# Kernel tuning notes

Measured on AMD Instinct MI355X. Metric: run time of the kernel, lower is better.

Reference implementation:

```python
import jax, jax.numpy as jnp
import numpy as np

CH = 128
DQK = CH // 8  # 16


def setup_inputs() -> dict:
    key = jax.random.key(0)
    ks = jax.random.split(key, 8)
    B, H, W, C = 4, 64, 64, CH
    inputs = jax.random.normal(ks[0], (B, H, W, C), dtype=jnp.float32)
    # 1x1 conv weights == dense over channel dim
    wq = jax.random.normal(ks[1], (C, DQK), dtype=jnp.float32) * (1.0 / np.sqrt(C))
    bq = jnp.zeros((DQK,), dtype=jnp.float32)
    wk = jax.random.normal(ks[2], (C, DQK), dtype=jnp.float32) * (1.0 / np.sqrt(C))
    bk = jnp.zeros((DQK,), dtype=jnp.float32)
    wv = jax.random.normal(ks[3], (C, C), dtype=jnp.float32) * (1.0 / np.sqrt(C))
    bv = jnp.zeros((C,), dtype=jnp.float32)
    gamma = jnp.zeros((1,), dtype=jnp.float32)
    return {"inputs": inputs, "wq": wq, "bq": bq, "wk": wk, "bk": bk,
            "wv": wv, "bv": bv, "gamma": gamma}


def reference(inputs, wq, bq, wk, bk, wv, bv, gamma):
    B, H, W, C = inputs.shape
    N = H * W
    x = inputs.reshape(B, N, C)  # flatten spatial
    q = x @ wq + bq              # [B, N, d]
    k = x @ wk + bk              # [B, N, d]
    v = x @ wv + bv              # [B, N, C]
    # full N x N attention (no scaling, per SAGAN source)
    scores = jnp.einsum('bnd,bmd->bnm', q, k)
    attn = jax.nn.softmax(scores, axis=-1)
    out = jnp.einsum('bnm,bmc->bnc', attn, v).reshape(B, H, W, C)
    return gamma * out + inputs
```

## Files before the change

kernel.cpp:

```cpp
#include <hip/hip_runtime.h>
#include <hip/hip_bf16.h>


typedef __attribute__((ext_vector_type(4)))  short short4v;
typedef __attribute__((ext_vector_type(8)))  short short8;
typedef __attribute__((ext_vector_type(16))) float f32x16;
typedef unsigned short u16;

#define LOG2E 1.4426950408889634f

__device__ __forceinline__ u16 f2bf(float f) {
  __hip_bfloat16 h = __float2bfloat16(f);
  return __builtin_bit_cast(u16, h);
}
__device__ __forceinline__ u16 f2bf_fast(float f) {
  unsigned u = __builtin_bit_cast(unsigned, f) + 0x8000u;
  return (u16)(u >> 16);
}
__device__ __forceinline__ float bf2f(u16 u) {
  unsigned v = (unsigned)u << 16;
  return __builtin_bit_cast(float, v);
}
__device__ __forceinline__ float fexp2(float x) {
#if __has_builtin(__builtin_amdgcn_exp2f)
  return __builtin_amdgcn_exp2f(x);
#else
  return exp2f(x);
#endif
}
__device__ __forceinline__ unsigned pkbf(float lo, float hi) {
  unsigned a = __builtin_bit_cast(unsigned, lo) + 0x8000u;
  unsigned b = __builtin_bit_cast(unsigned, hi) + 0x8000u;
  unsigned r;
  asm("v_perm_b32 %0, %1, %2, %3" : "=v"(r) : "v"(b), "v"(a), "s"(0x07060302u));
  return r;
}
__device__ __forceinline__ float xhalf_sum(float x) {
  float a = x, b = x;
  asm("v_permlane32_swap_b32 %0, %1" : "+v"(a), "+v"(b));
  return a + b;
}

__global__ __launch_bounds__(256) void qkv_proj(
    const float* __restrict__ x,
    const float* __restrict__ wq, const float* __restrict__ bq,
    const float* __restrict__ wk, const float* __restrict__ bk,
    const float* __restrict__ wv, const float* __restrict__ bv,
    u16* __restrict__ Qb, u16* __restrict__ Kb, u16* __restrict__ Vt)
{
  __shared__ u16 xs[128 * 136];
  __shared__ u16 ws[160 * 136];
  const int tid  = threadIdx.x;
  const int b    = blockIdx.x >> 6;
  const int n0   = ((blockIdx.x >> 1) & 31) * 128;
  const int half = blockIdx.x & 1;

  const float4* xg = (const float4*)(x + ((size_t)b * 4096 + n0) * 128);
#pragma unroll
  for (int p = 0; p < 16; ++p) {
    int idx = tid + p * 256;
    float4 v = xg[idx];
    int n = idx >> 5, i4 = idx & 31;
    short4v pk;
    pk[0] = (short)f2bf(v.x); pk[1] = (short)f2bf(v.y);
    pk[2] = (short)f2bf(v.z); pk[3] = (short)f2bf(v.w);
    *(short4v*)(xs + n * 136 + i4 * 4) = pk;
  }
  if (half == 0) {
#pragma unroll
    for (int p = 0; p < 8; ++p) {
      int idx = tid + p * 256;
      int k = idx >> 4, d = idx & 15;
      ws[d * 136 + k]        = f2bf(wq[idx] * LOG2E);
      ws[(16 + d) * 136 + k] = f2bf(wk[idx]);
    }
#pragma unroll
    for (int p = 0; p < 32; ++p) {
      int idx = tid + p * 256;
      int k = idx >> 6, c = idx & 63;
      ws[(32 + c) * 136 + k] = f2bf(wv[k * 128 + c]);
    }
  } else {
#pragma unroll
    for (int p = 0; p < 32; ++p) {
      int idx = tid + p * 256;
      int k = idx >> 6, c = 64 + (idx & 63);
      ws[(32 + c) * 136 + k] = f2bf(wv[k * 128 + c]);
    }
  }
  __syncthreads();

  const int lane = tid & 63, wid = tid >> 6;
  const int ln31 = lane & 31, hi = lane >> 5;
  const int NJ = half ? 2 : 3;

#pragma unroll 1
  for (int j = 0; j < NJ; ++j) {
    int t = wid + j * 4;
    int mt, nt;
    if (half == 0) { mt = t / 3; nt = t % 3; }
    else           { mt = t >> 1; nt = 3 + (t & 1); }
    const u16* arow = xs + (mt * 32 + ln31) * 136 + hi * 8;
    const u16* brow = ws + (nt * 32 + ln31) * 136 + hi * 8;
    f32x16 acc = (f32x16)0.0f;
#pragma unroll
    for (int ks = 0; ks < 8; ++ks) {
      short8 a = *(const short8*)(arow + ks * 16);
      short8 w = *(const short8*)(brow + ks * 16);
      acc = __builtin_amdgcn_mfma_f32_32x32x16_bf16(a, w, acc, 0, 0, 0);
    }
    if (nt == 0) {
      float bias = (ln31 < 16) ? bq[ln31] * LOG2E : bk[ln31 & 15];
      u16* base = ((ln31 < 16) ? Qb : Kb)
                + ((size_t)b * 4096 + n0 + mt * 32) * 16 + (ln31 & 15);
#pragma unroll
      for (int r = 0; r < 16; ++r) {
        int nl = (r & 3) + 8 * (r >> 2) + 4 * hi;
        base[nl * 16] = f2bf(acc[r] + bias);
      }
    } else {
      int c = (nt - 1) * 32 + ln31;
      float bias = bv[c];
      u16* vb = Vt + ((size_t)b * 128 + c) * 4096 + n0 + mt * 32 + 4 * hi;
#pragma unroll
      for (int g = 0; g < 4; ++g) {
        short4v pk;
        pk[0] = (short)f2bf(acc[g*4+0] + bias);
        pk[1] = (short)f2bf(acc[g*4+1] + bias);
        pk[2] = (short)f2bf(acc[g*4+2] + bias);
        pk[3] = (short)f2bf(acc[g*4+3] + bias);
        *(short4v*)(vb + 8 * g) = pk;
      }
    }
  }
}

template<int NKS>
__global__ __launch_bounds__(256, 3) void attn(
    const u16* __restrict__ Qb, const u16* __restrict__ Kb,
    const u16* __restrict__ Vt,
    u16* __restrict__ Ob, float* __restrict__ Lp)
{
  __shared__ __align__(16) char sm[2][18432];
  const int tid  = threadIdx.x;
  const int lane = tid & 63;
  const int wid  = tid >> 6;
  const int ln31 = lane & 31;
  const int hi   = lane >> 5;

  const int bx   = blockIdx.x;
  const int ks   = bx % NKS;
  const int rest = bx / NKS;
  const int b    = rest >> 5;
  const int qt   = rest & 31;
  const int qw   = qt * 128 + wid * 32;
  const int c0   = (ks * 64) / NKS;
  const int c1   = ((ks + 1) * 64) / NKS;

  const short8 qf = *(const short8*)(Qb + (((size_t)b * 4096 + qw + ln31) << 4) + (hi << 3));

  f32x16 acc[4];
#pragma unroll
  for (int ct = 0; ct < 4; ++ct) acc[ct] = (f32x16)0.0f;
  float lacc = 0.f;
  const f32x16 cbias = (f32x16)(-16.0f);

  const char* vg = (const char*)(Vt + (size_t)b * 128 * 4096);
  const char* kg = (const char*)(Kb + (size_t)b * 4096 * 16);
  const int vc = tid >> 1;
  const int vp = tid & 1;

  uint4 rv0, rv1, rv2, rv3;
  uint4 rk0, rk1;
  short8 paA0, paA1, paB0, paB1;

  auto loadV = [&](int kb) {
    const char* vs = vg + (size_t)vc * 8192 + (size_t)kb * 2 + vp * 64;
    rv0 = *(const uint4*)(vs);
    rv1 = *(const uint4*)(vs + 16);
    rv2 = *(const uint4*)(vs + 32);
    rv3 = *(const uint4*)(vs + 48);
  };
  auto loadK = [&](int kb) {
    const char* kr = kg + (size_t)(kb + ln31) * 32 + hi * 16;
    rk0 = *(const uint4*)(kr);
    rk1 = *(const uint4*)(kr + 1024);
  };
  auto storeV = [&](char* buf) {
    char* vd = buf + vc * 144 + vp * 64;
    *(uint4*)(vd)      = rv0;
    *(uint4*)(vd + 16) = rv1;
    *(uint4*)(vd + 32) = rv2;
    *(uint4*)(vd + 48) = rv3;
  };

  auto computeP = [&]() {
#pragma unroll
    for (int kt = 0; kt < 2; ++kt) {
      short8 kf = __builtin_bit_cast(short8, kt ? rk1 : rk0);
      f32x16 s = __builtin_amdgcn_mfma_f32_32x32x16_bf16(kf, qf, cbias, 0, 0, 0);

      float e0 = fexp2(s[0]),  e1 = fexp2(s[1]);
      unsigned u0 = pkbf(e0, e1);  float t0 = e0 + e1;
      float e2 = fexp2(s[2]),  e3 = fexp2(s[3]);
      unsigned u1 = pkbf(e2, e3);  float t1 = e2 + e3;
      float e4 = fexp2(s[4]),  e5 = fexp2(s[5]);
      unsigned u2 = pkbf(e4, e5);  float t2 = e4 + e5;
      float e6 = fexp2(s[6]),  e7 = fexp2(s[7]);
      unsigned u3 = pkbf(e6, e7);  float t3 = e6 + e7;
      float e8 = fexp2(s[8]),  e9 = fexp2(s[9]);
      unsigned y0 = pkbf(e8, e9);  float t4 = e8 + e9;
      float ea = fexp2(s[10]), eb = fexp2(s[11]);
      unsigned y1 = pkbf(ea, eb);  float t5 = ea + eb;
      float ec = fexp2(s[12]), ed = fexp2(s[13]);
      unsigned y2 = pkbf(ec, ed);  float t6 = ec + ed;
      float ee = fexp2(s[14]), ef = fexp2(s[15]);
      unsigned y3 = pkbf(ee, ef);  float t7 = ee + ef;
      lacc += ((t0 + t1) + (t2 + t3)) + ((t4 + t5) + (t6 + t7));

      asm("v_permlane32_swap_b32 %0, %1" : "+v"(u0), "+v"(u2));
      asm("v_permlane32_swap_b32 %0, %1" : "+v"(u1), "+v"(u3));
      asm("v_permlane32_swap_b32 %0, %1" : "+v"(y0), "+v"(y2));
      asm("v_permlane32_swap_b32 %0, %1" : "+v"(y1), "+v"(y3));
      union { unsigned u[4]; short8 s8; } f0, f1;
      f0.u[0] = u0; f0.u[1] = u1; f0.u[2] = u2; f0.u[3] = u3;
      f1.u[0] = y0; f1.u[1] = y1; f1.u[2] = y2; f1.u[3] = y3;
      if (kt == 0) { paA0 = f0.s8; paA1 = f1.s8; }
      else         { paB0 = f0.s8; paB1 = f1.s8; }
    }
  };

  auto doPV = [&](const char* buf) {
    __builtin_amdgcn_s_setprio(1);
#pragma unroll
    for (int ct = 0; ct < 4; ++ct) {
      const char* vrow = buf + (ct * 32 + ln31) * 144 + hi * 16;
      short8 v00 = *(const short8*)(vrow);
      short8 v01 = *(const short8*)(vrow + 32);
      short8 v10 = *(const short8*)(vrow + 64);
      short8 v11 = *(const short8*)(vrow + 96);
      acc[ct] = __builtin_amdgcn_mfma_f32_32x32x16_bf16(paA0, v00, acc[ct], 0, 0, 0);
      acc[ct] = __builtin_amdgcn_mfma_f32_32x32x16_bf16(paA1, v01, acc[ct], 0, 0, 0);
      acc[ct] = __builtin_amdgcn_mfma_f32_32x32x16_bf16(paB0, v10, acc[ct], 0, 0, 0);
      acc[ct] = __builtin_amdgcn_mfma_f32_32x32x16_bf16(paB1, v11, acc[ct], 0, 0, 0);
    }
    __builtin_amdgcn_s_setprio(0);
  };

  loadV(c0 * 64);
  loadK(c0 * 64);
  storeV(sm[0]);
  __syncthreads();
  computeP();
  int cur = 0;
#pragma unroll 1
  for (int it = c0; it < c1; ++it) {
    if (it < c1 - 1) {
      loadV((it + 1) * 64);
      loadK((it + 1) * 64);
    }
    doPV(sm[cur]);
    if (it < c1 - 1) {
      storeV(sm[cur ^ 1]);
      __syncthreads();
      computeP();
    }
    cur ^= 1;
  }

  float lt = xhalf_sum(lacc);
  if (lane < 32)
    Lp[(size_t)ks * 16384 + (size_t)b * 4096 + qw + lane] = lt;
  u16* Op = Ob + ((size_t)ks * 16384 + (size_t)b * 4096 + qw) * 128;
#pragma unroll
  for (int ct = 0; ct < 4; ++ct) {
#pragma unroll
    for (int r = 0; r < 16; ++r) {
      int q = (r & 3) + 8 * (r >> 2) + 4 * hi;
      Op[(size_t)q * 128 + ct * 32 + ln31] = f2bf_fast(acc[ct][r]);
    }
  }
}

template<int NKS>
__global__ __launch_bounds__(256) void combine(
    const u16* __restrict__ Ob, const float* __restrict__ Lp,
    const float* __restrict__ x, const float* __restrict__ gamma,
    float* __restrict__ out)
{
  int i    = blockIdx.x * 256 + threadIdx.x;
  int nrow = i >> 4;
  int c0   = (i & 15) << 3;

  float wsum = 0.f;
#pragma unroll
  for (int p = 0; p < NKS; ++p) wsum += Lp[(size_t)p * 16384 + nrow];
  float inv = gamma[0] / wsum;

  size_t off = (size_t)nrow * 128 + c0;
  float accv[8];
#pragma unroll
  for (int j = 0; j < 8; ++j) accv[j] = 0.f;
#pragma unroll
  for (int p = 0; p < NKS; ++p) {
    short8 v = *(const short8*)(Ob + (size_t)p * 16384 * 128 + off);
#pragma unroll
    for (int j = 0; j < 8; ++j) accv[j] += bf2f((u16)v[j]);
  }
  float4 xa = *(const float4*)(x + off);
  float4 xb = *(const float4*)(x + off + 4);
  float4 ra, rb;
  ra.x = fmaf(accv[0], inv, xa.x); ra.y = fmaf(accv[1], inv, xa.y);
  ra.z = fmaf(accv[2], inv, xa.z); ra.w = fmaf(accv[3], inv, xa.w);
  rb.x = fmaf(accv[4], inv, xb.x); rb.y = fmaf(accv[5], inv, xb.y);
  rb.z = fmaf(accv[6], inv, xb.z); rb.w = fmaf(accv[7], inv, xb.w);
  *(float4*)(out + off)     = ra;
  *(float4*)(out + off + 4) = rb;
}

extern "C" void kernel_launch(void* const* d_in, const int* in_sizes, int n_in,
                              void* d_out, int out_size, void* d_ws, size_t ws_size,
                              hipStream_t stream)
{
  const float* x  = (const float*)d_in[0];
  const float* wq = (const float*)d_in[1];
  const float* bq = (const float*)d_in[2];
  const float* wk = (const float*)d_in[3];
  const float* bk = (const float*)d_in[4];
  const float* wv = (const float*)d_in[5];
  const float* bv = (const float*)d_in[6];
  const float* gm = (const float*)d_in[7];

  char* w = (char*)d_ws;
  u16*   Qb = (u16*)(w);
  u16*   Kb = (u16*)(w + (512ll << 10));
  u16*   Vt = (u16*)(w + (1ll << 20));
  u16*   Ob = (u16*)(w + (5ll << 20));
  float* out = (float*)d_out;

  qkv_proj<<<256, 256, 0, stream>>>(x, wq, bq, wk, bk, wv, bv, Qb, Kb, Vt);

  const size_t need6 = (5ll << 20) + 6ll * (4ll << 20) + 6ll * 16384 * 4;
  if (ws_size >= need6) {
    float* Lp = (float*)(w + (5ll << 20) + 6ll * (4ll << 20));
    attn<6><<<768, 256, 0, stream>>>(Qb, Kb, Vt, Ob, Lp);
    combine<6><<<1024, 256, 0, stream>>>(Ob, Lp, x, gm, out);
  } else {
    float* Lp = (float*)(w + (5ll << 20) + 2ll * (4ll << 20));
    attn<2><<<256, 256, 0, stream>>>(Qb, Kb, Vt, Ob, Lp);
    combine<2><<<1024, 256, 0, stream>>>(Ob, Lp, x, gm, out);
  }
}
```

Before: 46.40 us.

## Stage V tiles via direct global-to-LDS loads with XOR swizzle; split keys 8 ways

V tiles now go straight from global memory into shared memory with global_load_lds, instead of passing through registers and a separate store. The padded row layout is replaced by an XOR-swizzled 128-byte layout to avoid bank conflicts without padding, and shared memory per block shrinks. Register pressure and the VGPR-to-LDS store step are removed. The key-split factor also goes from 6 to 8, with a 4-way fallback, giving more blocks but more partial outputs for the combine step to read.

```diff
diff --git a/kernel.cpp b/kernel.cpp
--- a/kernel.cpp
+++ b/kernel.cpp
@@ -8,6 +8,11 @@
 typedef unsigned short u16;
 
 #define LOG2E 1.4426950408889634f
+
+#define GLOAD_LDS16(g, l)                                                     \
+  __builtin_amdgcn_global_load_lds(                                           \
+      (const __attribute__((address_space(1))) void*)(g),                     \
+      (__attribute__((address_space(3))) void*)(l), 16, 0, 0)
 
 __device__ __forceinline__ u16 f2bf(float f) {
   __hip_bfloat16 h = __float2bfloat16(f);
@@ -141,7 +146,7 @@
     const u16* __restrict__ Vt,
     u16* __restrict__ Ob, float* __restrict__ Lp)
 {
-  __shared__ __align__(16) char sm[2][18432];
+  __shared__ __align__(16) char sm[2][16384];
   const int tid  = threadIdx.x;
   const int lane = tid & 63;
   const int wid  = tid >> 6;
@@ -165,33 +170,25 @@
   float lacc = 0.f;
   const f32x16 cbias = (f32x16)(-16.0f);
 
-  const char* vg = (const char*)(Vt + (size_t)b * 128 * 4096);
   const char* kg = (const char*)(Kb + (size_t)b * 4096 * 16);
-  const int vc = tid >> 1;
-  const int vp = tid & 1;
-
-  uint4 rv0, rv1, rv2, rv3;
+  const char* vsrc = (const char*)(Vt + (size_t)b * 128 * 4096)
+                   + (size_t)(wid * 32 + (lane >> 3)) * 8192
+                   + (((lane & 7) ^ (lane >> 3)) << 4);
+
   uint4 rk0, rk1;
   short8 paA0, paA1, paB0, paB1;
 
-  auto loadV = [&](int kb) {
-    const char* vs = vg + (size_t)vc * 8192 + (size_t)kb * 2 + vp * 64;
-    rv0 = *(const uint4*)(vs);
-    rv1 = *(const uint4*)(vs + 16);
-    rv2 = *(const uint4*)(vs + 32);
-    rv3 = *(const uint4*)(vs + 48);
+  auto stageV = [&](char* buf, int ck) {
+    char* ldst = buf + wid * 4096 + (lane << 4);
+    const char* g = vsrc + (size_t)ck * 128;
+#pragma unroll
+    for (int c = 0; c < 4; ++c)
+      GLOAD_LDS16(g + c * 65536, ldst + c * 1024);
   };
   auto loadK = [&](int kb) {
     const char* kr = kg + (size_t)(kb + ln31) * 32 + hi * 16;
     rk0 = *(const uint4*)(kr);
     rk1 = *(const uint4*)(kr + 1024);
-  };
-  auto storeV = [&](char* buf) {
-    char* vd = buf + vc * 144 + vp * 64;
-    *(uint4*)(vd)      = rv0;
-    *(uint4*)(vd + 16) = rv1;
-    *(uint4*)(vd + 32) = rv2;
-    *(uint4*)(vd + 48) = rv3;
   };
 
   auto computeP = [&]() {
@@ -231,14 +228,15 @@
   };
 
   auto doPV = [&](const char* buf) {
+    const int sw = ln31 & 7;
     __builtin_amdgcn_s_setprio(1);
 #pragma unroll
     for (int ct = 0; ct < 4; ++ct) {
-      const char* vrow = buf + (ct * 32 + ln31) * 144 + hi * 16;
-      short8 v00 = *(const short8*)(vrow);
-      short8 v01 = *(const short8*)(vrow + 32);
-      short8 v10 = *(const short8*)(vrow + 64);
-      short8 v11 = *(const short8*)(vrow + 96);
+      const char* vrow = buf + ct * 4096 + ln31 * 128;
+      short8 v00 = *(const short8*)(vrow + (((hi)     ^ sw) << 4));
+      short8 v01 = *(const short8*)(vrow + (((hi + 2) ^ sw) << 4));
+      short8 v10 = *(const short8*)(vrow + (((hi + 4) ^ sw) << 4));
+      short8 v11 = *(const short8*)(vrow + (((hi + 6) ^ sw) << 4));
       acc[ct] = __builtin_amdgcn_mfma_f32_32x32x16_bf16(paA0, v00, acc[ct], 0, 0, 0);
       acc[ct] = __builtin_amdgcn_mfma_f32_32x32x16_bf16(paA1, v01, acc[ct], 0, 0, 0);
       acc[ct] = __builtin_amdgcn_mfma_f32_32x32x16_bf16(paB0, v10, acc[ct], 0, 0, 0);
@@ -247,21 +245,19 @@
     __builtin_amdgcn_s_setprio(0);
   };
 
-  loadV(c0 * 64);
+  stageV(sm[0], c0);
   loadK(c0 * 64);
-  storeV(sm[0]);
   __syncthreads();
   computeP();
   int cur = 0;
 #pragma unroll 1
   for (int it = c0; it < c1; ++it) {
     if (it < c1 - 1) {
-      loadV((it + 1) * 64);
+      stageV(sm[cur ^ 1], it + 1);
       loadK((it + 1) * 64);
     }
     doPV(sm[cur]);
     if (it < c1 - 1) {
-      storeV(sm[cur ^ 1]);
       __syncthreads();
       computeP();
     }
@@ -340,11 +336,16 @@
 
   qkv_proj<<<256, 256, 0, stream>>>(x, wq, bq, wk, bk, wv, bv, Qb, Kb, Vt);
 
-  const size_t need6 = (5ll << 20) + 6ll * (4ll << 20) + 6ll * 16384 * 4;
-  if (ws_size >= need6) {
-    float* Lp = (float*)(w + (5ll << 20) + 6ll * (4ll << 20));
-    attn<6><<<768, 256, 0, stream>>>(Qb, Kb, Vt, Ob, Lp);
-    combine<6><<<1024, 256, 0, stream>>>(Ob, Lp, x, gm, out);
+  const size_t need8 = (5ll << 20) + 8ll * (4ll << 20) + 8ll * 16384 * 4;
+  const size_t need4 = (5ll << 20) + 4ll * (4ll << 20) + 4ll * 16384 * 4;
+  if (ws_size >= need8) {
+    float* Lp = (float*)(w + (5ll << 20) + 8ll * (4ll << 20));
+    attn<8><<<1024, 256, 0, stream>>>(Qb, Kb, Vt, Ob, Lp);
+    combine<8><<<1024, 256, 0, stream>>>(Ob, Lp, x, gm, out);
+  } else if (ws_size >= need4) {
+    float* Lp = (float*)(w + (5ll << 20) + 4ll * (4ll << 20));
+    attn<4><<<512, 256, 0, stream>>>(Qb, Kb, Vt, Ob, Lp);
+    combine<4><<<1024, 256, 0, stream>>>(Ob, Lp, x, gm, out);
   } else {
     float* Lp = (float*)(w + (5ll << 20) + 2ll * (4ll << 20));
     attn<2><<<256, 256, 0, stream>>>(Qb, Kb, Vt, Ob, Lp);
```

Result: slower. 50.05 us (+7.9%).
